# Performance work log

Hardware: AMD Instinct MI355X
Metric: run time of the kernel (lower is better)

## Reference

```python
import jax, jax.numpy as jnp
import numpy as np

N_NODES = 100000
N_EDGES = 1600000
N_FEAT = 128
HIDDEN = 128
N_GRAPHS = 1024


def setup_inputs() -> dict:
    key = jax.random.key(0)
    ks = jax.random.split(key, 9)
    x = jax.random.normal(ks[0], (N_NODES, N_FEAT), dtype=jnp.float32)
    edge_index = jax.random.randint(ks[1], (2, N_EDGES), 0, N_NODES, dtype=jnp.int64)
    batch = jnp.sort(jax.random.randint(ks[2], (N_NODES,), 0, N_GRAPHS, dtype=jnp.int64))
    W1 = jax.random.normal(ks[3], (N_FEAT, HIDDEN), dtype=jnp.float32) * (1.0 / np.sqrt(N_FEAT))
    b1 = jax.random.normal(ks[4], (HIDDEN,), dtype=jnp.float32) * 0.01
    W2 = jax.random.normal(ks[5], (HIDDEN, HIDDEN), dtype=jnp.float32) * (1.0 / np.sqrt(HIDDEN))
    b2 = jax.random.normal(ks[6], (HIDDEN,), dtype=jnp.float32) * 0.01
    Wl = jax.random.normal(ks[7], (HIDDEN, 2), dtype=jnp.float32) * (1.0 / np.sqrt(HIDDEN))
    bl = jax.random.normal(ks[8], (2,), dtype=jnp.float32) * 0.01
    return {"x": x, "edge_index": edge_index, "batch": batch,
            "W1": W1, "b1": b1, "W2": W2, "b2": b2, "Wl": Wl, "bl": bl}


def _gcn_norm(edge_index, num_nodes):
    # PyG GCNConv: add self-loops, then sym-normalize with in-degree (target col).
    loop = jnp.arange(num_nodes, dtype=edge_index.dtype)
    src = jnp.concatenate([edge_index[0], loop])  # [E+N]
    dst = jnp.concatenate([edge_index[1], loop])  # [E+N]
    deg = jax.ops.segment_sum(jnp.ones_like(dst, dtype=jnp.float32), dst,
                              num_segments=num_nodes)
    dinv = jnp.where(deg > 0, jax.lax.rsqrt(deg), 0.0)
    norm = dinv[src] * dinv[dst]  # [E+N]
    return src, dst, norm


def _gcn_conv(h, W, b, src, dst, norm, num_nodes):
    h = h @ W                                   # [N, out]
    msg = h[src] * norm[:, None]                # gather + scale, [E+N, out]
    agg = jax.ops.segment_sum(msg, dst, num_segments=num_nodes)  # scatter-add
    return agg + b


def reference(x, edge_index, batch, W1, b1, W2, b2, Wl, bl):
    n = x.shape[0]
    src, dst, norm = _gcn_norm(edge_index, n)
    h = jax.nn.relu(_gcn_conv(x, W1, b1, src, dst, norm, n))
    h = jax.nn.relu(_gcn_conv(h, W2, b2, src, dst, norm, n))
    # global_mean_pool over graph ids
    sums = jax.ops.segment_sum(h, batch, num_segments=N_GRAPHS)        # [G, H]
    counts = jax.ops.segment_sum(jnp.ones((n,), jnp.float32), batch,
                                 num_segments=N_GRAPHS)
    pooled = sums / jnp.maximum(counts, 1.0)[:, None]
    # F.dropout with training=False default in inference -> identity
    return pooled @ Wl + bl  # [G, 2]
```

## Files before the change

### kernel.cpp

```cpp
#include <hip/hip_runtime.h>
#include <hip/hip_bf16.h>

#define N_NODES 100000
#define N_EDGES 1600000
#define FEAT 128
#define N_GRAPHS 1024
#define NBUCK 391
#define CHUNK 4096
#define NT128 782
#define G1A 391
#define G1B 391

typedef short short8 __attribute__((ext_vector_type(8)));
typedef float float4v __attribute__((ext_vector_type(4)));

static __device__ inline unsigned short f2bf(float f) {
    __hip_bfloat16 b = __float2bfloat16(f);
    unsigned short r;
    __builtin_memcpy(&r, &b, 2);
    return r;
}
static __device__ inline float bf_lo(unsigned int v) { return __uint_as_float(v << 16); }
static __device__ inline float bf_hi(unsigned int v) { return __uint_as_float(v & 0xFFFF0000u); }

__global__ __launch_bounds__(256) void k_prep_hist(const float* __restrict__ W1,
                                                   const float* __restrict__ W2,
                                                   unsigned short* __restrict__ wp1,
                                                   unsigned short* __restrict__ wp2,
                                                   const int* __restrict__ dst,
                                                   int* __restrict__ bcount,
                                                   unsigned int* __restrict__ udummy,
                                                   unsigned int* __restrict__ u2dummy,
                                                   float* __restrict__ dinv) {
    int bid = blockIdx.x;
    if (bid < 128) {
        const float* W = (bid < 64) ? W1 : W2;
        unsigned short* wp = (bid < 64) ? wp1 : wp2;
        int t = (bid & 63) * 256 + threadIdx.x;
        int k = t >> 7, n = t & 127;
        float w = W[k * 128 + n];
        unsigned ub = __float_as_uint(w);
        unsigned short hi = (unsigned short)(ub >> 16);
        float hif = __uint_as_float(ub & 0xFFFF0000u);
        unsigned short lo = f2bf(w - hif);
        int sidx = n * 128 + ((k & 7) | (8 * (((k >> 3) ^ n) & 15)));
        wp[sidx] = hi;
        wp[16384 + sidx] = lo;
        if (bid == 0) {
            if (threadIdx.x < 64) udummy[threadIdx.x] = 0;
            else if (threadIdx.x < 128) u2dummy[threadIdx.x - 64] = 0;
            else if (threadIdx.x == 128) dinv[N_NODES] = 0.f;
        }
    } else {
        __shared__ int h[NBUCK];
        for (int i = threadIdx.x; i < NBUCK; i += 256) h[i] = 0;
        __syncthreads();
        int hb = bid - 128;
        for (int e = hb * 256 + threadIdx.x; e < N_EDGES; e += 256 * 256)
            atomicAdd(&h[dst[e] >> 8], 1);
        __syncthreads();
        for (int i = threadIdx.x; i < NBUCK; i += 256) {
            int c = h[i];
            if (c) atomicAdd(&bcount[i], c);
        }
    }
}

__global__ __launch_bounds__(512) void k_scan391(const int* __restrict__ in,
                                                 int* __restrict__ base,
                                                 int* __restrict__ cur,
                                                 int* __restrict__ tail) {
    int t = threadIdx.x;
    int v = (t < NBUCK) ? in[t] : 0;
    int lane = t & 63, wid = t >> 6;
    int s = v;
#pragma unroll
    for (int d = 1; d < 64; d <<= 1) { int n = __shfl_up(s, d); if (lane >= d) s += n; }
    __shared__ int ws[8];
    if (lane == 63) ws[wid] = s;
    __syncthreads();
    if (t < 8) {
        int x = ws[t];
#pragma unroll
        for (int d = 1; d < 8; d <<= 1) { int n = __shfl_up(x, d); if ((int)t >= d) x += n; }
        ws[t] = x;
    }
    __syncthreads();
    int excl = s - v + (wid ? ws[wid - 1] : 0);
    if (t < NBUCK) {
        base[t] = excl;
        cur[t] = excl;
    }
    if (t == 0) tail[0] = N_EDGES;
}

__device__ __forceinline__ void gemm_f32_body(int tile, const float* __restrict__ inp,
                                              const unsigned short* __restrict__ wp,
                                              unsigned short* __restrict__ u) {
    __shared__ unsigned short sW[32768];
    {
        float4* d4 = (float4*)sW;
        const float4* s4 = (const float4*)wp;
#pragma unroll
        for (int i = 0; i < 16; ++i) d4[threadIdx.x + 256 * i] = s4[threadIdx.x + 256 * i];
    }
    __syncthreads();
    const int t = threadIdx.x;
    const int w = t >> 6, L = t & 63;
    const int m = L & 15, q = L >> 4;
    const int r0 = tile * 128 + w * 32;
    int ar0 = r0 + m;
    int ar1 = r0 + 16 + m;
    if (ar0 >= N_NODES) ar0 = N_NODES - 1;
    if (ar1 >= N_NODES) ar1 = N_NODES - 1;
    const float4* ap0 = (const float4*)(inp + (size_t)ar0 * 128);
    const float4* ap1 = (const float4*)(inp + (size_t)ar1 * 128);
    float4v acc0[8], acc1[8];
#pragma unroll
    for (int c = 0; c < 8; ++c) {
        acc0[c] = (float4v){0.f, 0.f, 0.f, 0.f};
        acc1[c] = (float4v){0.f, 0.f, 0.f, 0.f};
    }
#pragma unroll
    for (int k0 = 0; k0 < 128; k0 += 32) {
        short8 ah0, al0, ah1, al1;
        {
            float4 f0 = ap0[(k0 >> 2) + 2 * q];
            float4 f1 = ap0[(k0 >> 2) + 2 * q + 1];
            float fa[8] = {f0.x, f0.y, f0.z, f0.w, f1.x, f1.y, f1.z, f1.w};
#pragma unroll
            for (int j = 0; j < 8; ++j) {
                unsigned ub = __float_as_uint(fa[j]);
                ah0[j] = (short)(ub >> 16);
                float hif = __uint_as_float(ub & 0xFFFF0000u);
                al0[j] = (short)f2bf(fa[j] - hif);
            }
        }
        {
            float4 f0 = ap1[(k0 >> 2) + 2 * q];
            float4 f1 = ap1[(k0 >> 2) + 2 * q + 1];
            float fa[8] = {f0.x, f0.y, f0.z, f0.w, f1.x, f1.y, f1.z, f1.w};
#pragma unroll
            for (int j = 0; j < 8; ++j) {
                unsigned ub = __float_as_uint(fa[j]);
                ah1[j] = (short)(ub >> 16);
                float hif = __uint_as_float(ub & 0xFFFF0000u);
                al1[j] = (short)f2bf(fa[j] - hif);
            }
        }
        const int b = (k0 >> 3) + q;
#pragma unroll
        for (int c = 0; c < 8; ++c) {
            int ng = c * 16 + m;
            int elem = ng * 128 + 8 * ((b ^ ng) & 15);
            short8 bh = *(const short8*)&sW[elem];
            short8 bl = *(const short8*)&sW[16384 + elem];
            acc0[c] = __builtin_amdgcn_mfma_f32_16x16x32_bf16(ah0, bh, acc0[c], 0, 0, 0);
            acc0[c] = __builtin_amdgcn_mfma_f32_16x16x32_bf16(al0, bh, acc0[c], 0, 0, 0);
            acc0[c] = __builtin_amdgcn_mfma_f32_16x16x32_bf16(ah0, bl, acc0[c], 0, 0, 0);
            acc1[c] = __builtin_amdgcn_mfma_f32_16x16x32_bf16(ah1, bh, acc1[c], 0, 0, 0);
            acc1[c] = __builtin_amdgcn_mfma_f32_16x16x32_bf16(al1, bh, acc1[c], 0, 0, 0);
            acc1[c] = __builtin_amdgcn_mfma_f32_16x16x32_bf16(ah1, bl, acc1[c], 0, 0, 0);
        }
    }
#pragma unroll
    for (int r = 0; r < 4; ++r) {
        int row0 = r0 + 4 * q + r;
        if (row0 < N_NODES) {
            unsigned short* up = u + (size_t)row0 * 128 + m;
#pragma unroll
            for (int c = 0; c < 8; ++c) up[c * 16] = f2bf(acc0[c][r]);
        }
        int row1 = r0 + 16 + 4 * q + r;
        if (row1 < N_NODES) {
            unsigned short* up = u + (size_t)row1 * 128 + m;
#pragma unroll
            for (int c = 0; c < 8; ++c) up[c * 16] = f2bf(acc1[c][r]);
        }
    }
}

__global__ __launch_bounds__(256) void k_bucket_g1(const int* __restrict__ src,
                                                   const int* __restrict__ dst,
                                                   int* __restrict__ bcur,
                                                   unsigned int* __restrict__ pairs,
                                                   const float* __restrict__ x,
                                                   const unsigned short* __restrict__ wp1,
                                                   unsigned short* __restrict__ u) {
    if (blockIdx.x >= NBUCK) {
        gemm_f32_body(blockIdx.x - NBUCK, x, wp1, u);
        return;
    }
    __shared__ int cnt[NBUCK];
    __shared__ int basebuf[NBUCK];
    int t = threadIdx.x;
    int e0 = blockIdx.x * CHUNK;
    for (int i = t; i < NBUCK; i += 256) cnt[i] = 0;
    __syncthreads();
    unsigned pk[16]; int bk[16];
#pragma unroll
    for (int j = 0; j < 16; ++j) {
        int e = e0 + j * 256 + t;
        if (e < N_EDGES) {
            int s = src[e], d = dst[e];
            bk[j] = d >> 8;
            pk[j] = ((unsigned)s << 8) | (unsigned)(d & 255);
            atomicAdd(&cnt[bk[j]], 1);
        } else bk[j] = -1;
    }
    __syncthreads();
    for (int i = t; i < NBUCK; i += 256) {
        int c = cnt[i];
        basebuf[i] = c ? atomicAdd(&bcur[i], c) : 0;
        cnt[i] = 0;
    }
    __syncthreads();
#pragma unroll
    for (int j = 0; j < 16; ++j) {
        if (bk[j] >= 0) {
            int p = basebuf[bk[j]] + atomicAdd(&cnt[bk[j]], 1);
            pairs[p] = pk[j];
        }
    }
}

__global__ __launch_bounds__(256) void k_bfill_g1(const unsigned int* __restrict__ pairs,
                                                  const int* __restrict__ bbase,
                                                  const int* __restrict__ bcount,
                                                  float* __restrict__ dinv,
                                                  int* __restrict__ offs,
                                                  int* __restrict__ csr,
                                                  const float* __restrict__ x,
                                                  const unsigned short* __restrict__ wp1,
                                                  unsigned short* __restrict__ u) {
    if (blockIdx.x >= NBUCK) {
        gemm_f32_body(blockIdx.x - NBUCK + G1A, x, wp1, u);
        return;
    }
    __shared__ int degl[256];
    __shared__ int lcur[256];
    __shared__ int ws[4];
    int b = blockIdx.x, t = threadIdx.x;
    degl[t] = 0;
    __syncthreads();
    int s0 = bbase[b], n = bcount[b];
    for (int i = t; i < n; i += 256) atomicAdd(&degl[pairs[s0 + i] & 255u], 1);
    __syncthreads();
    int node = b * 256 + t;
    int dv = degl[t];
    if (node < N_NODES) dinv[node] = rsqrtf((float)(dv + 1));
    int lane = t & 63, wid = t >> 6;
    int s = dv;
#pragma unroll
    for (int d = 1; d < 64; d <<= 1) { int nn = __shfl_up(s, d); if (lane >= d) s += nn; }
    if (lane == 63) ws[wid] = s;
    __syncthreads();
    if (t < 4) {
        int xx = ws[t];
#pragma unroll
        for (int d = 1; d < 4; d <<= 1) { int nn = __shfl_up(xx, d); if ((int)t >= d) xx += nn; }
        ws[t] = xx;
    }
    __syncthreads();
    int excl = s - dv + (wid ? ws[wid - 1] : 0) + bbase[b];
    if (node < N_NODES) offs[node] = excl;
    lcur[t] = excl;
    __syncthreads();
    for (int i = t; i < n; i += 256) {
        unsigned pr = pairs[s0 + i];
        int p = atomicAdd(&lcur[pr & 255u], 1);
        csr[p] = (int)(pr >> 8);
    }
}

__global__ __launch_bounds__(256, 8) void k_agg1_g2(const unsigned int* __restrict__ u,
                                                    const int* __restrict__ offs,
                                                    const int* __restrict__ csr,
                                                    const float* __restrict__ dinv,
                                                    const float* __restrict__ bias,
                                                    const unsigned short* __restrict__ wp,
                                                    unsigned short* __restrict__ u2) {
    __shared__ float hS[16 * 128];
    const int w = threadIdx.x >> 6;
    const int lane = threadIdx.x & 63;
    const int base = blockIdx.x * 16;

    for (int n = 0; n < 4; ++n) {
        const int row = 4 * w + n;
        const int node = base + row;
        int p = __builtin_amdgcn_readfirstlane(offs[node]);
        int e = __builtin_amdgcn_readfirstlane(offs[node + 1]);
        float dsf = dinv[node];
        unsigned int self = u[(size_t)node * 64 + lane];
        float ax0 = dsf * bf_lo(self), ay0 = dsf * bf_hi(self);
        float ax1 = 0.f, ay1 = 0.f, ax2 = 0.f, ay2 = 0.f, ax3 = 0.f, ay3 = 0.f;
        float ax4 = 0.f, ay4 = 0.f, ax5 = 0.f, ay5 = 0.f, ax6 = 0.f, ay6 = 0.f;
        float ax7 = 0.f, ay7 = 0.f;
        for (; p < e; p += 8) {
            int c0 = csr[p + 0], c1 = csr[p + 1], c2 = csr[p + 2], c3 = csr[p + 3];
            int c4 = csr[p + 4], c5 = csr[p + 5], c6 = csr[p + 6], c7 = csr[p + 7];
            int i0 = c0;
            int i1 = (p + 1 < e) ? c1 : N_NODES;
            int i2 = (p + 2 < e) ? c2 : N_NODES;
            int i3 = (p + 3 < e) ? c3 : N_NODES;
            int i4 = (p + 4 < e) ? c4 : N_NODES;
            int i5 = (p + 5 < e) ? c5 : N_NODES;
            int i6 = (p + 6 < e) ? c6 : N_NODES;
            int i7 = (p + 7 < e) ? c7 : N_NODES;
            float d0 = dinv[i0], d1 = dinv[i1], d2 = dinv[i2], d3 = dinv[i3];
            float d4 = dinv[i4], d5 = dinv[i5], d6 = dinv[i6], d7 = dinv[i7];
            unsigned v0 = (u + (size_t)i0 * 64)[lane];
            unsigned v1 = (u + (size_t)i1 * 64)[lane];
            unsigned v2 = (u + (size_t)i2 * 64)[lane];
            unsigned v3 = (u + (size_t)i3 * 64)[lane];
            unsigned v4 = (u + (size_t)i4 * 64)[lane];
            unsigned v5 = (u + (size_t)i5 * 64)[lane];
            unsigned v6 = (u + (size_t)i6 * 64)[lane];
            unsigned v7 = (u + (size_t)i7 * 64)[lane];
            ax0 = fmaf(d0, bf_lo(v0), ax0); ay0 = fmaf(d0, bf_hi(v0), ay0);
            ax1 = fmaf(d1, bf_lo(v1), ax1); ay1 = fmaf(d1, bf_hi(v1), ay1);
            ax2 = fmaf(d2, bf_lo(v2), ax2); ay2 = fmaf(d2, bf_hi(v2), ay2);
            ax3 = fmaf(d3, bf_lo(v3), ax3); ay3 = fmaf(d3, bf_hi(v3), ay3);
            ax4 = fmaf(d4, bf_lo(v4), ax4); ay4 = fmaf(d4, bf_hi(v4), ay4);
            ax5 = fmaf(d5, bf_lo(v5), ax5); ay5 = fmaf(d5, bf_hi(v5), ay5);
            ax6 = fmaf(d6, bf_lo(v6), ax6); ay6 = fmaf(d6, bf_hi(v6), ay6);
            ax7 = fmaf(d7, bf_lo(v7), ax7); ay7 = fmaf(d7, bf_hi(v7), ay7);
        }
        float2 b = ((const float2*)bias)[lane];
        float sx = ((ax0 + ax1) + (ax2 + ax3)) + ((ax4 + ax5) + (ax6 + ax7));
        float sy = ((ay0 + ay1) + (ay2 + ay3)) + ((ay4 + ay5) + (ay6 + ay7));
        float r0 = fmaxf(dsf * sx + b.x, 0.f);
        float r1 = fmaxf(dsf * sy + b.y, 0.f);
        int g4 = (lane >> 1) ^ (row & 7);
        float2* hp = (float2*)&hS[row * 128 + g4 * 4 + (lane & 1) * 2];
        *hp = (float2){r0, r1};
    }

    const int m = lane & 15, q = lane >> 4;
    const int cw = w;
    const int arow = m;
    const int ng0 = (2 * cw + 0) * 16 + m;
    const int ng1 = (2 * cw + 1) * 16 + m;
    short8 bh0, bl0, bh1, bl1;
    {
        int b = q;
        int e0 = ng0 * 128 + 8 * ((b ^ ng0) & 15);
        int e1 = ng1 * 128 + 8 * ((b ^ ng1) & 15);
        bh0 = *(const short8*)&wp[e0];
        bl0 = *(const short8*)&wp[16384 + e0];
        bh1 = *(const short8*)&wp[e1];
        bl1 = *(const short8*)&wp[16384 + e1];
    }
    __syncthreads();

    float4v acc0 = (float4v){0.f, 0.f, 0.f, 0.f};
    float4v acc1 = (float4v){0.f, 0.f, 0.f, 0.f};
#pragma unroll
    for (int ks = 0; ks < 4; ++ks) {
        short8 nh0, nl0, nh1, nl1;
        if (ks < 3) {
            int b = 4 * (ks + 1) + q;
            int e0 = ng0 * 128 + 8 * ((b ^ ng0) & 15);
            int e1 = ng1 * 128 + 8 * ((b ^ ng1) & 15);
            nh0 = *(const short8*)&wp[e0];
            nl0 = *(const short8*)&wp[16384 + e0];
            nh1 = *(const short8*)&wp[e1];
            nl1 = *(const short8*)&wp[16384 + e1];
        }
        const int k0 = 32 * ks;
        int g1 = (k0 >> 2) + 2 * q;
        float4 f0 = *(const float4*)&hS[arow * 128 + ((g1 ^ (arow & 7)) << 2)];
        float4 f1 = *(const float4*)&hS[arow * 128 + (((g1 + 1) ^ (arow & 7)) << 2)];
        float fa[8] = {f0.x, f0.y, f0.z, f0.w, f1.x, f1.y, f1.z, f1.w};
        short8 ah, al;
#pragma unroll
        for (int j = 0; j < 8; ++j) {
            unsigned ub = __float_as_uint(fa[j]);
            ah[j] = (short)(ub >> 16);
            float hif = __uint_as_float(ub & 0xFFFF0000u);
            al[j] = (short)f2bf(fa[j] - hif);
        }
        acc0 = __builtin_amdgcn_mfma_f32_16x16x32_bf16(ah, bh0, acc0, 0, 0, 0);
        acc0 = __builtin_amdgcn_mfma_f32_16x16x32_bf16(al, bh0, acc0, 0, 0, 0);
        acc0 = __builtin_amdgcn_mfma_f32_16x16x32_bf16(ah, bl0, acc0, 0, 0, 0);
        acc1 = __builtin_amdgcn_mfma_f32_16x16x32_bf16(ah, bh1, acc1, 0, 0, 0);
        acc1 = __builtin_amdgcn_mfma_f32_16x16x32_bf16(al, bh1, acc1, 0, 0, 0);
        acc1 = __builtin_amdgcn_mfma_f32_16x16x32_bf16(ah, bl1, acc1, 0, 0, 0);
        if (ks < 3) {
            bh0 = nh0; bl0 = nl0; bh1 = nh1; bl1 = nl1;
        }
    }
#pragma unroll
    for (int r = 0; r < 4; ++r) {
        int row = 4 * q + r;
        unsigned short* up = u2 + (size_t)(base + row) * 128 + m;
        up[(2 * cw + 0) * 16] = f2bf(acc0[r]);
        up[(2 * cw + 1) * 16] = f2bf(acc1[r]);
    }
}

__global__ __launch_bounds__(256) void k_agg2(const unsigned int* __restrict__ u,
                                              const int* __restrict__ offs,
                                              const int* __restrict__ csr,
                                              const float* __restrict__ dinv,
                                              const float* __restrict__ bias,
                                              const float* __restrict__ Wl,
                                              float* __restrict__ pnode) {
    int wid = threadIdx.x >> 6;
    int lane = threadIdx.x & 63;
    int node = __builtin_amdgcn_readfirstlane(blockIdx.x * 4 + wid);
    if (node >= N_NODES) return;
    int p = __builtin_amdgcn_readfirstlane(offs[node]);
    int e = __builtin_amdgcn_readfirstlane(offs[node + 1]);
    float dsf = dinv[node];
    unsigned int self = u[(size_t)node * 64 + lane];
    float ax0 = dsf * bf_lo(self), ay0 = dsf * bf_hi(self);
    float ax1 = 0.f, ay1 = 0.f, ax2 = 0.f, ay2 = 0.f, ax3 = 0.f, ay3 = 0.f;
    float ax4 = 0.f, ay4 = 0.f, ax5 = 0.f, ay5 = 0.f, ax6 = 0.f, ay6 = 0.f;
    float ax7 = 0.f, ay7 = 0.f;
    for (; p < e; p += 8) {
        int c0 = csr[p + 0], c1 = csr[p + 1], c2 = csr[p + 2], c3 = csr[p + 3];
        int c4 = csr[p + 4], c5 = csr[p + 5], c6 = csr[p + 6], c7 = csr[p + 7];
        int i0 = c0;
        int i1 = (p + 1 < e) ? c1 : N_NODES;
        int i2 = (p + 2 < e) ? c2 : N_NODES;
        int i3 = (p + 3 < e) ? c3 : N_NODES;
        int i4 = (p + 4 < e) ? c4 : N_NODES;
        int i5 = (p + 5 < e) ? c5 : N_NODES;
        int i6 = (p + 6 < e) ? c6 : N_NODES;
        int i7 = (p + 7 < e) ? c7 : N_NODES;
        float d0 = dinv[i0], d1 = dinv[i1], d2 = dinv[i2], d3 = dinv[i3];
        float d4 = dinv[i4], d5 = dinv[i5], d6 = dinv[i6], d7 = dinv[i7];
        unsigned v0 = (u + (size_t)i0 * 64)[lane];
        unsigned v1 = (u + (size_t)i1 * 64)[lane];
        unsigned v2 = (u + (size_t)i2 * 64)[lane];
        unsigned v3 = (u + (size_t)i3 * 64)[lane];
        unsigned v4 = (u + (size_t)i4 * 64)[lane];
        unsigned v5 = (u + (size_t)i5 * 64)[lane];
        unsigned v6 = (u + (size_t)i6 * 64)[lane];
        unsigned v7 = (u + (size_t)i7 * 64)[lane];
        ax0 = fmaf(d0, bf_lo(v0), ax0); ay0 = fmaf(d0, bf_hi(v0), ay0);
        ax1 = fmaf(d1, bf_lo(v1), ax1); ay1 = fmaf(d1, bf_hi(v1), ay1);
        ax2 = fmaf(d2, bf_lo(v2), ax2); ay2 = fmaf(d2, bf_hi(v2), ay2);
        ax3 = fmaf(d3, bf_lo(v3), ax3); ay3 = fmaf(d3, bf_hi(v3), ay3);
        ax4 = fmaf(d4, bf_lo(v4), ax4); ay4 = fmaf(d4, bf_hi(v4), ay4);
        ax5 = fmaf(d5, bf_lo(v5), ax5); ay5 = fmaf(d5, bf_hi(v5), ay5);
        ax6 = fmaf(d6, bf_lo(v6), ax6); ay6 = fmaf(d6, bf_hi(v6), ay6);
        ax7 = fmaf(d7, bf_lo(v7), ax7); ay7 = fmaf(d7, bf_hi(v7), ay7);
    }
    float2 b = ((const float2*)bias)[lane];
    float sx = ((ax0 + ax1) + (ax2 + ax3)) + ((ax4 + ax5) + (ax6 + ax7));
    float sy = ((ay0 + ay1) + (ay2 + ay3)) + ((ay4 + ay5) + (ay6 + ay7));
    float r0 = fmaxf(dsf * sx + b.x, 0.f);
    float r1 = fmaxf(dsf * sy + b.y, 0.f);
    float2 wl0 = ((const float2*)Wl)[2 * lane];
    float2 wl1 = ((const float2*)Wl)[2 * lane + 1];
    float p0 = r0 * wl0.x + r1 * wl1.x;
    float p1 = r0 * wl0.y + r1 * wl1.y;
#pragma unroll
    for (int d = 32; d > 0; d >>= 1) {
        p0 += __shfl_xor(p0, d);
        p1 += __shfl_xor(p1, d);
    }
    if (lane == 0) {
        float2* pp = (float2*)pnode;
        pp[node] = (float2){p0, p1};
    }
}

__global__ __launch_bounds__(64) void k_fin(const float* __restrict__ pnode,
                                            const int* __restrict__ batch,
                                            const float* __restrict__ bl,
                                            float* __restrict__ out) {
    int g = blockIdx.x;
    int lane = threadIdx.x;
    __shared__ int sb[2];
    if (lane < 2) {
        int tgt = g + lane;
        int lo = 0, hi = N_NODES;
        while (lo < hi) { int m = (lo + hi) >> 1; if (batch[m] < tgt) lo = m + 1; else hi = m; }
        sb[lane] = lo;
    }
    __syncthreads();
    int s0 = sb[0], s1 = sb[1];
    const float2* pp = (const float2*)pnode;
    float p0 = 0.f, p1 = 0.f;
    for (int i = s0 + lane; i < s1; i += 64) {
        float2 v = pp[i];
        p0 += v.x;
        p1 += v.y;
    }
#pragma unroll
    for (int d = 32; d > 0; d >>= 1) {
        p0 += __shfl_xor(p0, d);
        p1 += __shfl_xor(p1, d);
    }
    if (lane == 0) {
        float inv = 1.f / fmaxf((float)(s1 - s0), 1.f);
        out[2 * g + 0] = p0 * inv + bl[0];
        out[2 * g + 1] = p1 * inv + bl[1];
    }
}

extern "C" void kernel_launch(void* const* d_in, const int* in_sizes, int n_in,
                              void* d_out, int out_size, void* d_ws, size_t ws_size,
                              hipStream_t stream) {
    const float* x  = (const float*)d_in[0];
    const int* ei   = (const int*)d_in[1];
    const int* batch = (const int*)d_in[2];
    const float* W1 = (const float*)d_in[3];
    const float* b1 = (const float*)d_in[4];
    const float* W2 = (const float*)d_in[5];
    const float* b2 = (const float*)d_in[6];
    const float* Wl = (const float*)d_in[7];
    const float* bl = (const float*)d_in[8];
    float* out = (float*)d_out;
    const int* src = ei;
    const int* dst = ei + N_EDGES;

    char* ws = (char*)d_ws;
    size_t o = 0;
    auto alloc = [&](size_t bytes) -> void* {
        o = (o + 255) & ~(size_t)255;
        void* p = ws + o;
        o += bytes;
        return p;
    };
    int* bcount = (int*)alloc((size_t)NBUCK * 4);
    int* bbase  = (int*)alloc((size_t)NBUCK * 4);
    int* bcur   = (int*)alloc((size_t)NBUCK * 4);
    float* dinv = (float*)alloc((size_t)(N_NODES + 1) * 4);
    int* offs   = (int*)alloc((size_t)(N_NODES + 1) * 4);
    unsigned short* wp1 = (unsigned short*)alloc(65536);
    unsigned short* wp2 = (unsigned short*)alloc(65536);
    float* pnode = (float*)alloc((size_t)N_NODES * 2 * 4);
    unsigned int* pairs = (unsigned int*)alloc((size_t)N_EDGES * 4);
    int* csr    = (int*)alloc((size_t)(N_EDGES + 8) * 4);
    unsigned short* u  = (unsigned short*)alloc((size_t)(N_NODES + 1) * 128 * 2);
    unsigned short* u2 = (unsigned short*)alloc((size_t)(N_NODES + 1) * 128 * 2);

    hipMemsetAsync(bcount, 0, (size_t)NBUCK * 4, stream);
    k_prep_hist<<<384, 256, 0, stream>>>(W1, W2, wp1, wp2, dst, bcount,
                                         (unsigned int*)(u + (size_t)N_NODES * 128),
                                         (unsigned int*)(u2 + (size_t)N_NODES * 128), dinv);
    k_scan391<<<1, 512, 0, stream>>>(bcount, bbase, bcur, &offs[N_NODES]);
    k_bucket_g1<<<NBUCK + G1A, 256, 0, stream>>>(src, dst, bcur, pairs, x, wp1, u);
    k_bfill_g1<<<NBUCK + G1B, 256, 0, stream>>>(pairs, bbase, bcount, dinv, offs, csr, x, wp1, u);

    k_agg1_g2<<<N_NODES / 16, 256, 0, stream>>>((const unsigned int*)u, offs, csr, dinv, b1,
                                                wp2, u2);
    k_agg2<<<(N_NODES + 3) / 4, 256, 0, stream>>>((const unsigned int*)u2, offs, csr, dinv, b2,
                                                  Wl, pnode);

    k_fin<<<N_GRAPHS, 64, 0, stream>>>(pnode, batch, bl, out);
}
```

Before: 304.4 us.

## Compute node degrees in histogram pass and halve agg1 block size

```diff
diff --git a/kernel.cpp b/kernel.cpp
--- a/kernel.cpp
+++ b/kernel.cpp
@@ -29,6 +29,7 @@
                                                    unsigned short* __restrict__ wp2,
                                                    const int* __restrict__ dst,
                                                    int* __restrict__ bcount,
+                                                   int* __restrict__ deg,
                                                    unsigned int* __restrict__ udummy,
                                                    unsigned int* __restrict__ u2dummy,
                                                    float* __restrict__ dinv) {
@@ -56,8 +57,11 @@
         for (int i = threadIdx.x; i < NBUCK; i += 256) h[i] = 0;
         __syncthreads();
         int hb = bid - 128;
-        for (int e = hb * 256 + threadIdx.x; e < N_EDGES; e += 256 * 256)
-            atomicAdd(&h[dst[e] >> 8], 1);
+        for (int e = hb * 256 + threadIdx.x; e < N_EDGES; e += 256 * 256) {
+            int d = dst[e];
+            atomicAdd(&h[d >> 8], 1);
+            atomicAdd(&deg[d], 1);
+        }
         __syncthreads();
         for (int i = threadIdx.x; i < NBUCK; i += 256) {
             int c = h[i];
@@ -227,6 +231,7 @@
 __global__ __launch_bounds__(256) void k_bfill_g1(const unsigned int* __restrict__ pairs,
                                                   const int* __restrict__ bbase,
                                                   const int* __restrict__ bcount,
+                                                  const int* __restrict__ deg,
                                                   float* __restrict__ dinv,
                                                   int* __restrict__ offs,
                                                   int* __restrict__ csr,
@@ -237,17 +242,11 @@
         gemm_f32_body(blockIdx.x - NBUCK + G1A, x, wp1, u);
         return;
     }
-    __shared__ int degl[256];
     __shared__ int lcur[256];
     __shared__ int ws[4];
     int b = blockIdx.x, t = threadIdx.x;
-    degl[t] = 0;
-    __syncthreads();
-    int s0 = bbase[b], n = bcount[b];
-    for (int i = t; i < n; i += 256) atomicAdd(&degl[pairs[s0 + i] & 255u], 1);
-    __syncthreads();
     int node = b * 256 + t;
-    int dv = degl[t];
+    int dv = (node < N_NODES) ? deg[node] : 0;
     if (node < N_NODES) dinv[node] = rsqrtf((float)(dv + 1));
     int lane = t & 63, wid = t >> 6;
     int s = dv;
@@ -266,6 +265,7 @@
     if (node < N_NODES) offs[node] = excl;
     lcur[t] = excl;
     __syncthreads();
+    int s0 = bbase[b], n = bcount[b];
     for (int i = t; i < n; i += 256) {
         unsigned pr = pairs[s0 + i];
         int p = atomicAdd(&lcur[pr & 255u], 1);
@@ -273,7 +273,7 @@
     }
 }
 
-__global__ __launch_bounds__(256, 8) void k_agg1_g2(const unsigned int* __restrict__ u,
+__global__ __launch_bounds__(128, 8) void k_agg1_g2(const unsigned int* __restrict__ u,
                                                     const int* __restrict__ offs,
                                                     const int* __restrict__ csr,
                                                     const float* __restrict__ dinv,
@@ -285,8 +285,8 @@
     const int lane = threadIdx.x & 63;
     const int base = blockIdx.x * 16;
 
-    for (int n = 0; n < 4; ++n) {
-        const int row = 4 * w + n;
+    for (int n = 0; n < 8; ++n) {
+        const int row = 8 * w + n;
         const int node = base + row;
         int p = __builtin_amdgcn_readfirstlane(offs[node]);
         int e = __builtin_amdgcn_readfirstlane(offs[node + 1]);
@@ -335,67 +335,53 @@
         float2* hp = (float2*)&hS[row * 128 + g4 * 4 + (lane & 1) * 2];
         *hp = (float2){r0, r1};
     }
+    __syncthreads();
 
     const int m = lane & 15, q = lane >> 4;
-    const int cw = w;
     const int arow = m;
-    const int ng0 = (2 * cw + 0) * 16 + m;
-    const int ng1 = (2 * cw + 1) * 16 + m;
-    short8 bh0, bl0, bh1, bl1;
-    {
-        int b = q;
-        int e0 = ng0 * 128 + 8 * ((b ^ ng0) & 15);
-        int e1 = ng1 * 128 + 8 * ((b ^ ng1) & 15);
-        bh0 = *(const short8*)&wp[e0];
-        bl0 = *(const short8*)&wp[16384 + e0];
-        bh1 = *(const short8*)&wp[e1];
-        bl1 = *(const short8*)&wp[16384 + e1];
-    }
-    __syncthreads();
-
-    float4v acc0 = (float4v){0.f, 0.f, 0.f, 0.f};
-    float4v acc1 = (float4v){0.f, 0.f, 0.f, 0.f};
-#pragma unroll
-    for (int ks = 0; ks < 4; ++ks) {
-        short8 nh0, nl0, nh1, nl1;
-        if (ks < 3) {
-            int b = 4 * (ks + 1) + q;
+#pragma unroll
+    for (int cp = 0; cp < 2; ++cp) {
+        const int cq = 2 * w + cp;
+        const int ng0 = (2 * cq + 0) * 16 + m;
+        const int ng1 = (2 * cq + 1) * 16 + m;
+        float4v acc0 = (float4v){0.f, 0.f, 0.f, 0.f};
+        float4v acc1 = (float4v){0.f, 0.f, 0.f, 0.f};
+#pragma unroll
+        for (int ks = 0; ks < 4; ++ks) {
+            const int k0 = 32 * ks;
+            int g1 = (k0 >> 2) + 2 * q;
+            float4 f0 = *(const float4*)&hS[arow * 128 + ((g1 ^ (arow & 7)) << 2)];
+            float4 f1 = *(const float4*)&hS[arow * 128 + (((g1 + 1) ^ (arow & 7)) << 2)];
+            float fa[8] = {f0.x, f0.y, f0.z, f0.w, f1.x, f1.y, f1.z, f1.w};
+            short8 ah, al;
+#pragma unroll
+            for (int j = 0; j < 8; ++j) {
+                unsigned ub = __float_as_uint(fa[j]);
+                ah[j] = (short)(ub >> 16);
+                float hif = __uint_as_float(ub & 0xFFFF0000u);
+                al[j] = (short)f2bf(fa[j] - hif);
+            }
+            const int b = 4 * ks + q;
             int e0 = ng0 * 128 + 8 * ((b ^ ng0) & 15);
             int e1 = ng1 * 128 + 8 * ((b ^ ng1) & 15);
-            nh0 = *(const short8*)&wp[e0];
-            nl0 = *(const short8*)&wp[16384 + e0];
-            nh1 = *(const short8*)&wp[e1];
-            nl1 = *(const short8*)&wp[16384 + e1];
-        }
-        const int k0 = 32 * ks;
-        int g1 = (k0 >> 2) + 2 * q;
-        float4 f0 = *(const float4*)&hS[arow * 128 + ((g1 ^ (arow & 7)) << 2)];
-        float4 f1 = *(const float4*)&hS[arow * 128 + (((g1 + 1) ^ (arow & 7)) << 2)];
-        float fa[8] = {f0.x, f0.y, f0.z, f0.w, f1.x, f1.y, f1.z, f1.w};
-        short8 ah, al;
-#pragma unroll
-        for (int j = 0; j < 8; ++j) {
-            unsigned ub = __float_as_uint(fa[j]);
-            ah[j] = (short)(ub >> 16);
-            float hif = __uint_as_float(ub & 0xFFFF0000u);
-            al[j] = (short)f2bf(fa[j] - hif);
-        }
-        acc0 = __builtin_amdgcn_mfma_f32_16x16x32_bf16(ah, bh0, acc0, 0, 0, 0);
-        acc0 = __builtin_amdgcn_mfma_f32_16x16x32_bf16(al, bh0, acc0, 0, 0, 0);
-        acc0 = __builtin_amdgcn_mfma_f32_16x16x32_bf16(ah, bl0, acc0, 0, 0, 0);
-        acc1 = __builtin_amdgcn_mfma_f32_16x16x32_bf16(ah, bh1, acc1, 0, 0, 0);
-        acc1 = __builtin_amdgcn_mfma_f32_16x16x32_bf16(al, bh1, acc1, 0, 0, 0);
-        acc1 = __builtin_amdgcn_mfma_f32_16x16x32_bf16(ah, bl1, acc1, 0, 0, 0);
-        if (ks < 3) {
-            bh0 = nh0; bl0 = nl0; bh1 = nh1; bl1 = nl1;
-        }
-    }
-#pragma unroll
-    for (int r = 0; r < 4; ++r) {
-        int row = 4 * q + r;
-        unsigned short* up = u2 + (size_t)(base + row) * 128 + m;
-        up[(2 * cw + 0) * 16] = f2bf(acc0[r]);
-        up[(2 * cw + 1) * 16] = f2bf(acc1[r]);
+            short8 bh0 = *(const short8*)&wp[e0];
+            short8 bl0 = *(const short8*)&wp[16384 + e0];
+            short8 bh1 = *(const short8*)&wp[e1];
+            short8 bl1 = *(const short8*)&wp[16384 + e1];
+            acc0 = __builtin_amdgcn_mfma_f32_16x16x32_bf16(ah, bh0, acc0, 0, 0, 0);
+            acc0 = __builtin_amdgcn_mfma_f32_16x16x32_bf16(al, bh0, acc0, 0, 0, 0);
+            acc0 = __builtin_amdgcn_mfma_f32_16x16x32_bf16(ah, bl0, acc0, 0, 0, 0);
+            acc1 = __builtin_amdgcn_mfma_f32_16x16x32_bf16(ah, bh1, acc1, 0, 0, 0);
+            acc1 = __builtin_amdgcn_mfma_f32_16x16x32_bf16(al, bh1, acc1, 0, 0, 0);
+            acc1 = __builtin_amdgcn_mfma_f32_16x16x32_bf16(ah, bl1, acc1, 0, 0, 0);
+        }
+#pragma unroll
+        for (int r = 0; r < 4; ++r) {
+            int row = 4 * q + r;
+            unsigned short* up = u2 + (size_t)(base + row) * 128 + m;
+            up[(2 * cq + 0) * 16] = f2bf(acc0[r]);
+            up[(2 * cq + 1) * 16] = f2bf(acc1[r]);
+        }
     }
 }
 
@@ -529,6 +515,7 @@
     int* bcount = (int*)alloc((size_t)NBUCK * 4);
     int* bbase  = (int*)alloc((size_t)NBUCK * 4);
     int* bcur   = (int*)alloc((size_t)NBUCK * 4);
+    int* deg    = (int*)alloc((size_t)N_NODES * 4);
     float* dinv = (float*)alloc((size_t)(N_NODES + 1) * 4);
     int* offs   = (int*)alloc((size_t)(N_NODES + 1) * 4);
     unsigned short* wp1 = (unsigned short*)alloc(65536);
@@ -540,14 +527,16 @@
     unsigned short* u2 = (unsigned short*)alloc((size_t)(N_NODES + 1) * 128 * 2);
 
     hipMemsetAsync(bcount, 0, (size_t)NBUCK * 4, stream);
-    k_prep_hist<<<384, 256, 0, stream>>>(W1, W2, wp1, wp2, dst, bcount,
+    hipMemsetAsync(deg, 0, (size_t)N_NODES * 4, stream);
+    k_prep_hist<<<384, 256, 0, stream>>>(W1, W2, wp1, wp2, dst, bcount, deg,
                                          (unsigned int*)(u + (size_t)N_NODES * 128),
                                          (unsigned int*)(u2 + (size_t)N_NODES * 128), dinv);
     k_scan391<<<1, 512, 0, stream>>>(bcount, bbase, bcur, &offs[N_NODES]);
     k_bucket_g1<<<NBUCK + G1A, 256, 0, stream>>>(src, dst, bcur, pairs, x, wp1, u);
-    k_bfill_g1<<<NBUCK + G1B, 256, 0, stream>>>(pairs, bbase, bcount, dinv, offs, csr, x, wp1, u);
-
-    k_agg1_g2<<<N_NODES / 16, 256, 0, stream>>>((const unsigned int*)u, offs, csr, dinv, b1,
+    k_bfill_g1<<<NBUCK + G1B, 256, 0, stream>>>(pairs, bbase, bcount, deg, dinv, offs, csr,
+                                                x, wp1, u);
+
+    k_agg1_g2<<<N_NODES / 16, 128, 0, stream>>>((const unsigned int*)u, offs, csr, dinv, b1,
                                                 wp2, u2);
     k_agg2<<<(N_NODES + 3) / 4, 256, 0, stream>>>((const unsigned int*)u2, offs, csr, dinv, b2,
                                                   Wl, pnode);
```

Measured after the change: 384.2 us. 1.26x slower.
